# Optimization experiments

Measured on AMD Instinct MI355X. Metric: run time of the kernel, lower is better.

Reference implementation:

```python
import jax, jax.numpy as jnp
import numpy as np

TAU = 1.0
EPS = 1e-06


def setup_inputs() -> dict:
    key = jax.random.key(0)
    batch = jax.random.normal(key, (8192, 256), dtype=jnp.float32)
    return {"batch": batch}


def reference(batch):
    n = batch.shape[0]
    half = n // 2
    # reorder: interleave first half and second half -> [x0, y0, x1, y1, ...]
    idx = jnp.stack([jnp.arange(half), jnp.arange(half) + half], axis=1).reshape(-1)
    x = batch[idx]                                   # [n, d]

    sim = x @ x.T                                    # [n, n] raw dot products
    norm = jnp.linalg.norm(x, axis=1, keepdims=True) # [n, 1]
    normmat = norm @ norm.T                          # [n, n]

    # denominator: zero the diagonal BEFORE exp (diag contributes exp(0)=1, as in torch code)
    mask = 1.0 - jnp.eye(n, dtype=x.dtype)
    den = jnp.sum(jnp.exp(mask * sim / (normmat + EPS) / TAU), axis=1)  # [n]

    # numerator: for row k, positive pair is (i, i+1) with i = 2*(k//2); no eps (faithful)
    i = (jnp.arange(n) // 2) * 2
    num = sim[i, i + 1] / normmat[i, i + 1]          # [n]

    loss = jnp.sum(-jnp.log(jnp.exp(num / TAU) / den)) / n
    return loss
```

## Files before the change

### kernel.cpp

```cpp
#include <hip/hip_runtime.h>
#include <hip/hip_bf16.h>


#define N_ROWS 8192
#define HALF   4096
#define DDIM   256
#define NBLK   64

typedef unsigned int   u32;
typedef unsigned char  u8;
typedef __attribute__((ext_vector_type(4))) float f32x4;
typedef __attribute__((ext_vector_type(4))) int   i32x4;
typedef __attribute__((ext_vector_type(8))) int   i32x8;

__device__ __forceinline__ u32 f2e4m3(float f) {
    const u32 u = __builtin_bit_cast(u32, f);
    const u32 s = (u >> 24) & 0x80u;
    const float af = fabsf(f);
    if (af < 0.015625f) {
        const int mi = (int)rintf(af * 512.0f);
        return s | (u32)mi;
    }
    u32 keep = (u & 0x7FFFFFFFu) >> 20;
    const u32 rem = u & 0xFFFFFu;
    keep += (rem > 0x80000u) || (rem == 0x80000u && (keep & 1u));
    const int ef = (int)(keep >> 3) - 120;
    return s | ((u32)ef << 3) | (keep & 7u);
}

__global__ __launch_bounds__(256) void prep_kernel(const float* __restrict__ x,
                                                   u8* __restrict__ xq,
                                                   float* __restrict__ norms,
                                                   float* __restrict__ dots) {
    const int w = threadIdx.x >> 6, l = threadIdx.x & 63;
    if (blockIdx.x < 2048) {
        const int row = blockIdx.x * 4 + w;
        const float4 v = reinterpret_cast<const float4*>(x + (size_t)row * DDIM)[l];
        float sq = v.x * v.x + v.y * v.y + v.z * v.z + v.w * v.w;
#pragma unroll
        for (int off = 1; off < 64; off <<= 1) sq += __shfl_xor(sq, off);
        const float norm = sqrtf(sq);
        if (l == 0) norms[row] = norm;
        const float rs = 16.0f / norm;
        const u32 pk = f2e4m3(v.x * rs) | (f2e4m3(v.y * rs) << 8) |
                       (f2e4m3(v.z * rs) << 16) | (f2e4m3(v.w * rs) << 24);
        reinterpret_cast<u32*>(xq + (size_t)row * DDIM)[l] = pk;
    } else {
        const int m = (blockIdx.x - 2048) * 4 + w;
        const float4 a = reinterpret_cast<const float4*>(x + (size_t)m * DDIM)[l];
        const float4 b = reinterpret_cast<const float4*>(x + (size_t)(m + HALF) * DDIM)[l];
        float s = a.x * b.x + a.y * b.y + a.z * b.z + a.w * b.w;
#pragma unroll
        for (int off = 1; off < 64; off <<= 1) s += __shfl_xor(s, off);
        if (l == 0) dots[m] = s;
    }
}

__global__ __launch_bounds__(256) void gram_kernel(const u8* __restrict__ xq,
                                                   float* __restrict__ part) {
    const int t = blockIdx.x;
    int bi = (int)(0.5f * (129.0f - sqrtf(16641.0f - 8.0f * (float)t)));
    if (bi > 0 && bi * (129 - bi) / 2 > t) --bi;
    if ((bi + 1) * (129 - (bi + 1)) / 2 <= t) ++bi;
    const int bj = bi + (t - bi * (129 - bi) / 2);
    const bool diagblk = (bi == bj);
    const int r0 = bi * 128, c0 = bj * 128;

    __shared__ __align__(16) char smem[32768];
    u8* As = (u8*)smem;
    u8* Bs = (u8*)(smem + 16384);

    const int tid = threadIdx.x;
    const int w = tid >> 6, l = tid & 63;
    const int wr = w >> 1, wc = w & 1;

    const f32x4 vzero = {0.f, 0.f, 0.f, 0.f};
    f32x4 acc[4][4];
#pragma unroll
    for (int m = 0; m < 4; ++m)
#pragma unroll
        for (int n = 0; n < 4; ++n) acc[m][n] = vzero;

    const int krow = l >> 3;
    const int kbyte = ((l & 7) ^ krow) * 16;
    const int r7 = l & 7;
    const int kq2 = (l >> 4) * 2;

    for (int ks = 0; ks < 2; ++ks) {
#pragma unroll
        for (int i = 0; i < 4; ++i) {
            const int rr = w * 32 + i * 8;
            const u8* ga = xq + (size_t)(r0 + rr + krow) * DDIM + ks * 128 + kbyte;
            __builtin_amdgcn_global_load_lds(
                (const __attribute__((address_space(1))) u32*)ga,
                (__attribute__((address_space(3))) u32*)(As + rr * 128), 16, 0, 0);
            const u8* gb = xq + (size_t)(c0 + rr + krow) * DDIM + ks * 128 + kbyte;
            __builtin_amdgcn_global_load_lds(
                (const __attribute__((address_space(1))) u32*)gb,
                (__attribute__((address_space(3))) u32*)(Bs + rr * 128), 16, 0, 0);
        }
        __syncthreads();

        i32x8 bfr[4];
#pragma unroll
        for (int m = 0; m < 4; ++m) {
            const u8* rowp = Bs + (wc * 64 + m * 16 + (l & 15)) * 128;
            const i32x4 lo = *reinterpret_cast<const i32x4*>(rowp + ((kq2 ^ r7) << 4));
            const i32x4 hi = *reinterpret_cast<const i32x4*>(rowp + (((kq2 + 1) ^ r7) << 4));
            bfr[m][0] = lo[0]; bfr[m][1] = lo[1]; bfr[m][2] = lo[2]; bfr[m][3] = lo[3];
            bfr[m][4] = hi[0]; bfr[m][5] = hi[1]; bfr[m][6] = hi[2]; bfr[m][7] = hi[3];
        }
#pragma unroll
        for (int n = 0; n < 4; ++n) {
            const u8* rowp = As + (wr * 64 + n * 16 + (l & 15)) * 128;
            const i32x4 lo = *reinterpret_cast<const i32x4*>(rowp + ((kq2 ^ r7) << 4));
            const i32x4 hi = *reinterpret_cast<const i32x4*>(rowp + (((kq2 + 1) ^ r7) << 4));
            i32x8 afr;
            afr[0] = lo[0]; afr[1] = lo[1]; afr[2] = lo[2]; afr[3] = lo[3];
            afr[4] = hi[0]; afr[5] = hi[1]; afr[6] = hi[2]; afr[7] = hi[3];
#pragma unroll
            for (int m = 0; m < 4; ++m)
                acc[m][n] = __builtin_amdgcn_mfma_scale_f32_16x16x128_f8f6f4(
                    bfr[m], afr, acc[m][n], 0, 0, 0, 0x7F7F7F7F, 0, 0x7F7F7F7F);
        }
        __syncthreads();
    }

#pragma unroll
    for (int m = 0; m < 4; ++m)
#pragma unroll
        for (int n = 0; n < 4; ++n)
#pragma unroll
            for (int rg = 0; rg < 4; ++rg) {
                const float e = __expf(acc[m][n][rg] * 0.00390625f);
                if (diagblk) {
                    const int j_loc = wc * 64 + m * 16 + (l >> 4) * 4 + rg;
                    const int r_loc = wr * 64 + n * 16 + (l & 15);
                    acc[m][n][rg] = (j_loc == r_loc) ? 1.0f : e;
                } else {
                    acc[m][n][rg] = e;
                }
            }

    float* cs  = (float*)smem;
    float* dsh = (float*)(smem + 24576);

#pragma unroll
    for (int n = 0; n < 4; ++n) {
        float s = 0.f;
#pragma unroll
        for (int m = 0; m < 4; ++m)
#pragma unroll
            for (int rg = 0; rg < 4; ++rg) s += acc[m][n][rg];
        s += __shfl_xor(s, 16);
        s += __shfl_xor(s, 32);
        if (l < 16) dsh[wc * 128 + wr * 64 + n * 16 + l] = s;
    }

    if (!diagblk) {
#pragma unroll
        for (int m = 0; m < 4; ++m)
#pragma unroll
            for (int rg = 0; rg < 4; ++rg) {
                const float s = acc[m][0][rg] + acc[m][1][rg] + acc[m][2][rg] + acc[m][3][rg];
                const int j_loc = wc * 64 + m * 16 + (l >> 4) * 4 + rg;
                cs[(wr * 128 + j_loc) * 17 + (l & 15)] = s;
            }
    }
    __syncthreads();

    if (tid < 128) {
        const float den = dsh[tid] + dsh[128 + tid];
        part[(size_t)bj * N_ROWS + r0 + tid] = den;
        if (!diagblk) {
            float c = 0.f;
#pragma unroll
            for (int k = 0; k < 16; ++k)
                c += cs[tid * 17 + k] + cs[(128 + tid) * 17 + k];
            part[(size_t)bi * N_ROWS + c0 + tid] = c;
        }
    }
}

__global__ __launch_bounds__(256) void fin1_kernel(const float* __restrict__ part,
                                                   const float* __restrict__ norms,
                                                   const float* __restrict__ dots,
                                                   float* __restrict__ bsum) {
    const int b = blockIdx.x, t = threadIdx.x;
    const int r = b * 256 + t;
    float den = 0.f;
#pragma unroll 8
    for (int bj = 0; bj < 64; ++bj) den += part[(size_t)bj * N_ROWS + r];
    float local = logf(den);
    if (t < 128) {
        const int m = b * 128 + t;
        local -= 2.0f * dots[m] / (norms[m] * norms[m + HALF]);
    }
#pragma unroll
    for (int off = 1; off < 64; off <<= 1) local += __shfl_xor(local, off);
    __shared__ float wsum[4];
    if ((t & 63) == 0) wsum[t >> 6] = local;
    __syncthreads();
    if (t == 0) bsum[b] = wsum[0] + wsum[1] + wsum[2] + wsum[3];
}

__global__ void fin2_kernel(const float* __restrict__ bsum, float* __restrict__ out) {
    const int t = threadIdx.x;
    float v = (t < 32) ? bsum[t] : 0.f;
#pragma unroll
    for (int off = 1; off < 32; off <<= 1) v += __shfl_xor(v, off);
    if (t == 0) out[0] = v / (float)N_ROWS;
}

extern "C" void kernel_launch(void* const* d_in, const int* in_sizes, int n_in,
                              void* d_out, int out_size, void* d_ws, size_t ws_size,
                              hipStream_t stream) {
    const float* x = (const float*)d_in[0];
    float* out = (float*)d_out;
    char* ws = (char*)d_ws;

    u8*    xq    = (u8*)ws;
    float* norms = (float*)(ws + 2097152);
    float* dots  = (float*)(ws + 2129920);
    float* part  = (float*)(ws + 2146304);
    float* bsum  = (float*)(ws + 4243456);

    prep_kernel<<<3072, 256, 0, stream>>>(x, xq, norms, dots);
    gram_kernel<<<(NBLK * (NBLK + 1)) / 2, 256, 0, stream>>>(xq, part);
    fin1_kernel<<<32, 256, 0, stream>>>(part, norms, dots, bsum);
    fin2_kernel<<<1, 64, 0, stream>>>(bsum, out);
}
```

Measured before the change: 34.11 us.

## Make gram kernel persistent over tile runs with double-buffered B staging

```diff
diff --git a/kernel.cpp b/kernel.cpp
--- a/kernel.cpp
+++ b/kernel.cpp
@@ -58,127 +58,175 @@
 
 __global__ __launch_bounds__(256) void gram_kernel(const u8* __restrict__ xq,
                                                    float* __restrict__ part) {
-    const int t = blockIdx.x;
-    int bi = (int)(0.5f * (129.0f - sqrtf(16641.0f - 8.0f * (float)t)));
-    if (bi > 0 && bi * (129 - bi) / 2 > t) --bi;
-    if ((bi + 1) * (129 - (bi + 1)) / 2 <= t) ++bi;
-    const int bj = bi + (t - bi * (129 - bi) / 2);
-    const bool diagblk = (bi == bj);
-    const int r0 = bi * 128, c0 = bj * 128;
-
-    __shared__ __align__(16) char smem[32768];
-    u8* As = (u8*)smem;
-    u8* Bs = (u8*)(smem + 16384);
+    const int b = blockIdx.x;
+    int tstart, tcnt;
+    if (b < 32) { tstart = 5 * b;      tcnt = 5; }
+    else        { tstart = 4 * b + 32; tcnt = 4; }
+
+    int bi = (int)(0.5f * (129.0f - sqrtf(16641.0f - 8.0f * (float)tstart)));
+    if (bi > 0 && bi * (129 - bi) / 2 > tstart) --bi;
+    if ((bi + 1) * (129 - (bi + 1)) / 2 <= tstart) ++bi;
+    int bj = bi + (tstart - bi * (129 - bi) / 2);
+
+    __shared__ __align__(16) char smem[51200];
+    float* cs  = (float*)(smem + 32768);
+    float* dsh = (float*)(smem + 32768 + 17408);
 
     const int tid = threadIdx.x;
     const int w = tid >> 6, l = tid & 63;
     const int wr = w >> 1, wc = w & 1;
-
-    const f32x4 vzero = {0.f, 0.f, 0.f, 0.f};
-    f32x4 acc[4][4];
-#pragma unroll
-    for (int m = 0; m < 4; ++m)
-#pragma unroll
-        for (int n = 0; n < 4; ++n) acc[m][n] = vzero;
 
     const int krow = l >> 3;
     const int kbyte = ((l & 7) ^ krow) * 16;
     const int r7 = l & 7;
     const int kq2 = (l >> 4) * 2;
 
-    for (int ks = 0; ks < 2; ++ks) {
+    auto stageB = [&](int c0, int ks, int bufsel) {
 #pragma unroll
         for (int i = 0; i < 4; ++i) {
             const int rr = w * 32 + i * 8;
-            const u8* ga = xq + (size_t)(r0 + rr + krow) * DDIM + ks * 128 + kbyte;
-            __builtin_amdgcn_global_load_lds(
-                (const __attribute__((address_space(1))) u32*)ga,
-                (__attribute__((address_space(3))) u32*)(As + rr * 128), 16, 0, 0);
             const u8* gb = xq + (size_t)(c0 + rr + krow) * DDIM + ks * 128 + kbyte;
             __builtin_amdgcn_global_load_lds(
                 (const __attribute__((address_space(1))) u32*)gb,
-                (__attribute__((address_space(3))) u32*)(Bs + rr * 128), 16, 0, 0);
-        }
+                (__attribute__((address_space(3))) u32*)((u8*)smem + bufsel * 16384 + rr * 128),
+                16, 0, 0);
+        }
+    };
+
+    i32x8 Areg[4][2];
+    f32x4 acc[4][4];
+
+    stageB(bj * 128, 0, 0);
+    int cur = 0;
+    bool newbi = true;
+
+    for (int tt = 0; tt < tcnt; ++tt) {
+        const bool diagblk = (bi == bj);
+        const int r0 = bi * 128, c0 = bj * 128;
+
+        int nbi = bi, nbj = bj + 1;
+        bool nnew = false;
+        if (nbj == NBLK) { nbi = bi + 1; nbj = nbi; nnew = true; }
+        const bool havenext = (tt + 1 < tcnt);
+
+        const f32x4 vzero = {0.f, 0.f, 0.f, 0.f};
+#pragma unroll
+        for (int m = 0; m < 4; ++m)
+#pragma unroll
+            for (int n = 0; n < 4; ++n) acc[m][n] = vzero;
+
         __syncthreads();
-
-        i32x8 bfr[4];
-#pragma unroll
-        for (int m = 0; m < 4; ++m) {
-            const u8* rowp = Bs + (wc * 64 + m * 16 + (l & 15)) * 128;
-            const i32x4 lo = *reinterpret_cast<const i32x4*>(rowp + ((kq2 ^ r7) << 4));
-            const i32x4 hi = *reinterpret_cast<const i32x4*>(rowp + (((kq2 + 1) ^ r7) << 4));
-            bfr[m][0] = lo[0]; bfr[m][1] = lo[1]; bfr[m][2] = lo[2]; bfr[m][3] = lo[3];
-            bfr[m][4] = hi[0]; bfr[m][5] = hi[1]; bfr[m][6] = hi[2]; bfr[m][7] = hi[3];
-        }
+        if (newbi) {
+#pragma unroll
+            for (int n = 0; n < 4; ++n)
+#pragma unroll
+                for (int ks = 0; ks < 2; ++ks) {
+                    const u8* ap = xq + (size_t)(r0 + wr * 64 + n * 16 + (l & 15)) * DDIM
+                                      + ks * 128 + (l >> 4) * 32;
+                    const i32x4 lo = *reinterpret_cast<const i32x4*>(ap);
+                    const i32x4 hi = *reinterpret_cast<const i32x4*>(ap + 16);
+                    Areg[n][ks][0] = lo[0]; Areg[n][ks][1] = lo[1];
+                    Areg[n][ks][2] = lo[2]; Areg[n][ks][3] = lo[3];
+                    Areg[n][ks][4] = hi[0]; Areg[n][ks][5] = hi[1];
+                    Areg[n][ks][6] = hi[2]; Areg[n][ks][7] = hi[3];
+                }
+        }
+        stageB(c0, 1, cur ^ 1);
+        {
+            const u8* Bsrc = (u8*)smem + cur * 16384;
+            i32x8 bfr[4];
+#pragma unroll
+            for (int m = 0; m < 4; ++m) {
+                const u8* rowp = Bsrc + (wc * 64 + m * 16 + (l & 15)) * 128;
+                const i32x4 lo = *reinterpret_cast<const i32x4*>(rowp + ((kq2 ^ r7) << 4));
+                const i32x4 hi = *reinterpret_cast<const i32x4*>(rowp + (((kq2 + 1) ^ r7) << 4));
+                bfr[m][0] = lo[0]; bfr[m][1] = lo[1]; bfr[m][2] = lo[2]; bfr[m][3] = lo[3];
+                bfr[m][4] = hi[0]; bfr[m][5] = hi[1]; bfr[m][6] = hi[2]; bfr[m][7] = hi[3];
+            }
+#pragma unroll
+            for (int n = 0; n < 4; ++n)
+#pragma unroll
+                for (int m = 0; m < 4; ++m)
+                    acc[m][n] = __builtin_amdgcn_mfma_scale_f32_16x16x128_f8f6f4(
+                        bfr[m], Areg[n][0], acc[m][n], 0, 0, 0, 0x7F7F7F7F, 0, 0x7F7F7F7F);
+        }
+        cur ^= 1;
+
+        __syncthreads();
+        if (havenext) stageB(nbj * 128, 0, cur ^ 1);
+        {
+            const u8* Bsrc = (u8*)smem + cur * 16384;
+            i32x8 bfr[4];
+#pragma unroll
+            for (int m = 0; m < 4; ++m) {
+                const u8* rowp = Bsrc + (wc * 64 + m * 16 + (l & 15)) * 128;
+                const i32x4 lo = *reinterpret_cast<const i32x4*>(rowp + ((kq2 ^ r7) << 4));
+                const i32x4 hi = *reinterpret_cast<const i32x4*>(rowp + (((kq2 + 1) ^ r7) << 4));
+                bfr[m][0] = lo[0]; bfr[m][1] = lo[1]; bfr[m][2] = lo[2]; bfr[m][3] = lo[3];
+                bfr[m][4] = hi[0]; bfr[m][5] = hi[1]; bfr[m][6] = hi[2]; bfr[m][7] = hi[3];
+            }
+#pragma unroll
+            for (int n = 0; n < 4; ++n)
+#pragma unroll
+                for (int m = 0; m < 4; ++m)
+                    acc[m][n] = __builtin_amdgcn_mfma_scale_f32_16x16x128_f8f6f4(
+                        bfr[m], Areg[n][1], acc[m][n], 0, 0, 0, 0x7F7F7F7F, 0, 0x7F7F7F7F);
+        }
+        cur ^= 1;
+
+#pragma unroll
+        for (int m = 0; m < 4; ++m)
+#pragma unroll
+            for (int n = 0; n < 4; ++n)
+#pragma unroll
+                for (int rg = 0; rg < 4; ++rg) {
+                    const float e = __expf(acc[m][n][rg] * 0.00390625f);
+                    if (diagblk) {
+                        const int j_loc = wc * 64 + m * 16 + (l >> 4) * 4 + rg;
+                        const int r_loc = wr * 64 + n * 16 + (l & 15);
+                        acc[m][n][rg] = (j_loc == r_loc) ? 1.0f : e;
+                    } else {
+                        acc[m][n][rg] = e;
+                    }
+                }
+
 #pragma unroll
         for (int n = 0; n < 4; ++n) {
-            const u8* rowp = As + (wr * 64 + n * 16 + (l & 15)) * 128;
-            const i32x4 lo = *reinterpret_cast<const i32x4*>(rowp + ((kq2 ^ r7) << 4));
-            const i32x4 hi = *reinterpret_cast<const i32x4*>(rowp + (((kq2 + 1) ^ r7) << 4));
-            i32x8 afr;
-            afr[0] = lo[0]; afr[1] = lo[1]; afr[2] = lo[2]; afr[3] = lo[3];
-            afr[4] = hi[0]; afr[5] = hi[1]; afr[6] = hi[2]; afr[7] = hi[3];
+            float s = 0.f;
 #pragma unroll
             for (int m = 0; m < 4; ++m)
-                acc[m][n] = __builtin_amdgcn_mfma_scale_f32_16x16x128_f8f6f4(
-                    bfr[m], afr, acc[m][n], 0, 0, 0, 0x7F7F7F7F, 0, 0x7F7F7F7F);
+#pragma unroll
+                for (int rg = 0; rg < 4; ++rg) s += acc[m][n][rg];
+            s += __shfl_xor(s, 16);
+            s += __shfl_xor(s, 32);
+            if (l < 16) dsh[wc * 128 + wr * 64 + n * 16 + l] = s;
+        }
+
+        if (!diagblk) {
+#pragma unroll
+            for (int m = 0; m < 4; ++m)
+#pragma unroll
+                for (int rg = 0; rg < 4; ++rg) {
+                    const float s = acc[m][0][rg] + acc[m][1][rg] + acc[m][2][rg] + acc[m][3][rg];
+                    const int j_loc = wc * 64 + m * 16 + (l >> 4) * 4 + rg;
+                    cs[(wr * 128 + j_loc) * 17 + (l & 15)] = s;
+                }
         }
         __syncthreads();
-    }
-
-#pragma unroll
-    for (int m = 0; m < 4; ++m)
-#pragma unroll
-        for (int n = 0; n < 4; ++n)
-#pragma unroll
-            for (int rg = 0; rg < 4; ++rg) {
-                const float e = __expf(acc[m][n][rg] * 0.00390625f);
-                if (diagblk) {
-                    const int j_loc = wc * 64 + m * 16 + (l >> 4) * 4 + rg;
-                    const int r_loc = wr * 64 + n * 16 + (l & 15);
-                    acc[m][n][rg] = (j_loc == r_loc) ? 1.0f : e;
-                } else {
-                    acc[m][n][rg] = e;
-                }
+
+        if (tid < 128) {
+            const float den = dsh[tid] + dsh[128 + tid];
+            part[(size_t)bj * N_ROWS + r0 + tid] = den;
+            if (!diagblk) {
+                float c = 0.f;
+#pragma unroll
+                for (int k = 0; k < 16; ++k)
+                    c += cs[tid * 17 + k] + cs[(128 + tid) * 17 + k];
+                part[(size_t)bi * N_ROWS + c0 + tid] = c;
             }
-
-    float* cs  = (float*)smem;
-    float* dsh = (float*)(smem + 24576);
-
-#pragma unroll
-    for (int n = 0; n < 4; ++n) {
-        float s = 0.f;
-#pragma unroll
-        for (int m = 0; m < 4; ++m)
-#pragma unroll
-            for (int rg = 0; rg < 4; ++rg) s += acc[m][n][rg];
-        s += __shfl_xor(s, 16);
-        s += __shfl_xor(s, 32);
-        if (l < 16) dsh[wc * 128 + wr * 64 + n * 16 + l] = s;
-    }
-
-    if (!diagblk) {
-#pragma unroll
-        for (int m = 0; m < 4; ++m)
-#pragma unroll
-            for (int rg = 0; rg < 4; ++rg) {
-                const float s = acc[m][0][rg] + acc[m][1][rg] + acc[m][2][rg] + acc[m][3][rg];
-                const int j_loc = wc * 64 + m * 16 + (l >> 4) * 4 + rg;
-                cs[(wr * 128 + j_loc) * 17 + (l & 15)] = s;
-            }
-    }
-    __syncthreads();
-
-    if (tid < 128) {
-        const float den = dsh[tid] + dsh[128 + tid];
-        part[(size_t)bj * N_ROWS + r0 + tid] = den;
-        if (!diagblk) {
-            float c = 0.f;
-#pragma unroll
-            for (int k = 0; k < 16; ++k)
-                c += cs[tid * 17 + k] + cs[(128 + tid) * 17 + k];
-            part[(size_t)bi * N_ROWS + c0 + tid] = c;
-        }
+        }
+
+        bi = nbi; bj = nbj; newbi = nnew;
     }
 }
 
@@ -226,7 +274,7 @@
     float* bsum  = (float*)(ws + 4243456);
 
     prep_kernel<<<3072, 256, 0, stream>>>(x, xq, norms, dots);
-    gram_kernel<<<(NBLK * (NBLK + 1)) / 2, 256, 0, stream>>>(xq, part);
+    gram_kernel<<<512, 256, 0, stream>>>(xq, part);
     fin1_kernel<<<32, 256, 0, stream>>>(part, norms, dots, bsum);
     fin2_kernel<<<1, 64, 0, stream>>>(bsum, out);
 }
```

Result: slower. 37.29 us (+9.3%).

## Load MFMA operand fragments directly from global into registers, dropping LDS staging

Applied to the files above, without the earlier changes.

```diff
diff --git a/kernel.cpp b/kernel.cpp
--- a/kernel.cpp
+++ b/kernel.cpp
@@ -66,14 +66,42 @@
     const bool diagblk = (bi == bj);
     const int r0 = bi * 128, c0 = bj * 128;
 
-    __shared__ __align__(16) char smem[32768];
-    u8* As = (u8*)smem;
-    u8* Bs = (u8*)(smem + 16384);
+    __shared__ float cs[2 * 128 * 17];
+    __shared__ float dsh[256];
 
     const int tid = threadIdx.x;
     const int w = tid >> 6, l = tid & 63;
     const int wr = w >> 1, wc = w & 1;
 
+    const u8* abase = xq + (size_t)(r0 + wr * 64 + (l & 15)) * DDIM + (l >> 4) * 32;
+    const u8* bbase = xq + (size_t)(c0 + wc * 64 + (l & 15)) * DDIM + (l >> 4) * 32;
+
+    i32x8 afr[4][2], bfr[4][2];
+#pragma unroll
+    for (int n = 0; n < 4; ++n)
+#pragma unroll
+        for (int ks = 0; ks < 2; ++ks) {
+            const u8* ap = abase + n * 16 * DDIM + ks * 128;
+            const i32x4 lo = *reinterpret_cast<const i32x4*>(ap);
+            const i32x4 hi = *reinterpret_cast<const i32x4*>(ap + 16);
+            afr[n][ks][0] = lo[0]; afr[n][ks][1] = lo[1];
+            afr[n][ks][2] = lo[2]; afr[n][ks][3] = lo[3];
+            afr[n][ks][4] = hi[0]; afr[n][ks][5] = hi[1];
+            afr[n][ks][6] = hi[2]; afr[n][ks][7] = hi[3];
+        }
+#pragma unroll
+    for (int m = 0; m < 4; ++m)
+#pragma unroll
+        for (int ks = 0; ks < 2; ++ks) {
+            const u8* bp = bbase + m * 16 * DDIM + ks * 128;
+            const i32x4 lo = *reinterpret_cast<const i32x4*>(bp);
+            const i32x4 hi = *reinterpret_cast<const i32x4*>(bp + 16);
+            bfr[m][ks][0] = lo[0]; bfr[m][ks][1] = lo[1];
+            bfr[m][ks][2] = lo[2]; bfr[m][ks][3] = lo[3];
+            bfr[m][ks][4] = hi[0]; bfr[m][ks][5] = hi[1];
+            bfr[m][ks][6] = hi[2]; bfr[m][ks][7] = hi[3];
+        }
+
     const f32x4 vzero = {0.f, 0.f, 0.f, 0.f};
     f32x4 acc[4][4];
 #pragma unroll
@@ -81,50 +109,14 @@
 #pragma unroll
         for (int n = 0; n < 4; ++n) acc[m][n] = vzero;
 
-    const int krow = l >> 3;
-    const int kbyte = ((l & 7) ^ krow) * 16;
-    const int r7 = l & 7;
-    const int kq2 = (l >> 4) * 2;
-
-    for (int ks = 0; ks < 2; ++ks) {
-#pragma unroll
-        for (int i = 0; i < 4; ++i) {
-            const int rr = w * 32 + i * 8;
-            const u8* ga = xq + (size_t)(r0 + rr + krow) * DDIM + ks * 128 + kbyte;
-            __builtin_amdgcn_global_load_lds(
-                (const __attribute__((address_space(1))) u32*)ga,
-                (__attribute__((address_space(3))) u32*)(As + rr * 128), 16, 0, 0);
-            const u8* gb = xq + (size_t)(c0 + rr + krow) * DDIM + ks * 128 + kbyte;
-            __builtin_amdgcn_global_load_lds(
-                (const __attribute__((address_space(1))) u32*)gb,
-                (__attribute__((address_space(3))) u32*)(Bs + rr * 128), 16, 0, 0);
-        }
-        __syncthreads();
-
-        i32x8 bfr[4];
-#pragma unroll
-        for (int m = 0; m < 4; ++m) {
-            const u8* rowp = Bs + (wc * 64 + m * 16 + (l & 15)) * 128;
-            const i32x4 lo = *reinterpret_cast<const i32x4*>(rowp + ((kq2 ^ r7) << 4));
-            const i32x4 hi = *reinterpret_cast<const i32x4*>(rowp + (((kq2 + 1) ^ r7) << 4));
-            bfr[m][0] = lo[0]; bfr[m][1] = lo[1]; bfr[m][2] = lo[2]; bfr[m][3] = lo[3];
-            bfr[m][4] = hi[0]; bfr[m][5] = hi[1]; bfr[m][6] = hi[2]; bfr[m][7] = hi[3];
-        }
-#pragma unroll
-        for (int n = 0; n < 4; ++n) {
-            const u8* rowp = As + (wr * 64 + n * 16 + (l & 15)) * 128;
-            const i32x4 lo = *reinterpret_cast<const i32x4*>(rowp + ((kq2 ^ r7) << 4));
-            const i32x4 hi = *reinterpret_cast<const i32x4*>(rowp + (((kq2 + 1) ^ r7) << 4));
-            i32x8 afr;
-            afr[0] = lo[0]; afr[1] = lo[1]; afr[2] = lo[2]; afr[3] = lo[3];
-            afr[4] = hi[0]; afr[5] = hi[1]; afr[6] = hi[2]; afr[7] = hi[3];
+#pragma unroll
+    for (int ks = 0; ks < 2; ++ks)
+#pragma unroll
+        for (int n = 0; n < 4; ++n)
 #pragma unroll
             for (int m = 0; m < 4; ++m)
                 acc[m][n] = __builtin_amdgcn_mfma_scale_f32_16x16x128_f8f6f4(
-                    bfr[m], afr, acc[m][n], 0, 0, 0, 0x7F7F7F7F, 0, 0x7F7F7F7F);
-        }
-        __syncthreads();
-    }
+                    bfr[m][ks], afr[n][ks], acc[m][n], 0, 0, 0, 0x7F7F7F7F, 0, 0x7F7F7F7F);
 
 #pragma unroll
     for (int m = 0; m < 4; ++m)
@@ -141,9 +133,6 @@
                     acc[m][n][rg] = e;
                 }
             }
-
-    float* cs  = (float*)smem;
-    float* dsh = (float*)(smem + 24576);
 
 #pragma unroll
     for (int n = 0; n < 4; ++n) {
```

Measured after the change: 52.08 us. 1.53x slower.

## Double-buffer Gram tile K-panels in LDS to overlap loads with MFMA

Applied to the files above, without the earlier changes.

```diff
diff --git a/kernel.cpp b/kernel.cpp
--- a/kernel.cpp
+++ b/kernel.cpp
@@ -66,45 +66,53 @@
     const bool diagblk = (bi == bj);
     const int r0 = bi * 128, c0 = bj * 128;
 
-    __shared__ __align__(16) char smem[32768];
-    u8* As = (u8*)smem;
-    u8* Bs = (u8*)(smem + 16384);
+    __shared__ __align__(16) u8 smem[65536];
+    u8* const A0 = smem;
+    u8* const A1 = smem + 16384;
+    u8* const B0 = smem + 32768;
+    u8* const B1 = smem + 49152;
 
     const int tid = threadIdx.x;
     const int w = tid >> 6, l = tid & 63;
     const int wr = w >> 1, wc = w & 1;
-
-    const f32x4 vzero = {0.f, 0.f, 0.f, 0.f};
-    f32x4 acc[4][4];
-#pragma unroll
-    for (int m = 0; m < 4; ++m)
-#pragma unroll
-        for (int n = 0; n < 4; ++n) acc[m][n] = vzero;
 
     const int krow = l >> 3;
     const int kbyte = ((l & 7) ^ krow) * 16;
     const int r7 = l & 7;
     const int kq2 = (l >> 4) * 2;
 
-    for (int ks = 0; ks < 2; ++ks) {
+    auto stage = [&](const u8* panel , int ks, u8* dst) {
 #pragma unroll
         for (int i = 0; i < 4; ++i) {
             const int rr = w * 32 + i * 8;
-            const u8* ga = xq + (size_t)(r0 + rr + krow) * DDIM + ks * 128 + kbyte;
+            const u8* g = panel + (size_t)(rr + krow) * DDIM + ks * 128 + kbyte;
             __builtin_amdgcn_global_load_lds(
-                (const __attribute__((address_space(1))) u32*)ga,
-                (__attribute__((address_space(3))) u32*)(As + rr * 128), 16, 0, 0);
-            const u8* gb = xq + (size_t)(c0 + rr + krow) * DDIM + ks * 128 + kbyte;
-            __builtin_amdgcn_global_load_lds(
-                (const __attribute__((address_space(1))) u32*)gb,
-                (__attribute__((address_space(3))) u32*)(Bs + rr * 128), 16, 0, 0);
-        }
-        __syncthreads();
-
-        i32x8 bfr[4];
+                (const __attribute__((address_space(1))) u32*)g,
+                (__attribute__((address_space(3))) u32*)(dst + rr * 128), 16, 0, 0);
+        }
+    };
+
+    const u8* apanel = xq + (size_t)r0 * DDIM;
+    const u8* bpanel = xq + (size_t)c0 * DDIM;
+
+    const f32x4 vzero = {0.f, 0.f, 0.f, 0.f};
+    f32x4 acc[4][4];
+#pragma unroll
+    for (int m = 0; m < 4; ++m)
+#pragma unroll
+        for (int n = 0; n < 4; ++n) acc[m][n] = vzero;
+
+    stage(apanel, 0, A0);
+    stage(apanel, 1, A1);
+    stage(bpanel, 0, B0);
+    __syncthreads();
+
+    stage(bpanel, 1, B1);
+    {
+        i32x8 afr[4], bfr[4];
 #pragma unroll
         for (int m = 0; m < 4; ++m) {
-            const u8* rowp = Bs + (wc * 64 + m * 16 + (l & 15)) * 128;
+            const u8* rowp = B0 + (wc * 64 + m * 16 + (l & 15)) * 128;
             const i32x4 lo = *reinterpret_cast<const i32x4*>(rowp + ((kq2 ^ r7) << 4));
             const i32x4 hi = *reinterpret_cast<const i32x4*>(rowp + (((kq2 + 1) ^ r7) << 4));
             bfr[m][0] = lo[0]; bfr[m][1] = lo[1]; bfr[m][2] = lo[2]; bfr[m][3] = lo[3];
@@ -112,18 +120,45 @@
         }
 #pragma unroll
         for (int n = 0; n < 4; ++n) {
-            const u8* rowp = As + (wr * 64 + n * 16 + (l & 15)) * 128;
-            const i32x4 lo = *reinterpret_cast<const i32x4*>(rowp + ((kq2 ^ r7) << 4));
-            const i32x4 hi = *reinterpret_cast<const i32x4*>(rowp + (((kq2 + 1) ^ r7) << 4));
-            i32x8 afr;
-            afr[0] = lo[0]; afr[1] = lo[1]; afr[2] = lo[2]; afr[3] = lo[3];
-            afr[4] = hi[0]; afr[5] = hi[1]; afr[6] = hi[2]; afr[7] = hi[3];
+            const u8* rowp = A0 + (wr * 64 + n * 16 + (l & 15)) * 128;
+            const i32x4 lo = *reinterpret_cast<const i32x4*>(rowp + ((kq2 ^ r7) << 4));
+            const i32x4 hi = *reinterpret_cast<const i32x4*>(rowp + (((kq2 + 1) ^ r7) << 4));
+            afr[n][0] = lo[0]; afr[n][1] = lo[1]; afr[n][2] = lo[2]; afr[n][3] = lo[3];
+            afr[n][4] = hi[0]; afr[n][5] = hi[1]; afr[n][6] = hi[2]; afr[n][7] = hi[3];
+        }
+#pragma unroll
+        for (int n = 0; n < 4; ++n)
 #pragma unroll
             for (int m = 0; m < 4; ++m)
                 acc[m][n] = __builtin_amdgcn_mfma_scale_f32_16x16x128_f8f6f4(
-                    bfr[m], afr, acc[m][n], 0, 0, 0, 0x7F7F7F7F, 0, 0x7F7F7F7F);
-        }
-        __syncthreads();
+                    bfr[m], afr[n], acc[m][n], 0, 0, 0, 0x7F7F7F7F, 0, 0x7F7F7F7F);
+    }
+    __syncthreads();
+
+    {
+        i32x8 afr[4], bfr[4];
+#pragma unroll
+        for (int m = 0; m < 4; ++m) {
+            const u8* rowp = B1 + (wc * 64 + m * 16 + (l & 15)) * 128;
+            const i32x4 lo = *reinterpret_cast<const i32x4*>(rowp + ((kq2 ^ r7) << 4));
+            const i32x4 hi = *reinterpret_cast<const i32x4*>(rowp + (((kq2 + 1) ^ r7) << 4));
+            bfr[m][0] = lo[0]; bfr[m][1] = lo[1]; bfr[m][2] = lo[2]; bfr[m][3] = lo[3];
+            bfr[m][4] = hi[0]; bfr[m][5] = hi[1]; bfr[m][6] = hi[2]; bfr[m][7] = hi[3];
+        }
+#pragma unroll
+        for (int n = 0; n < 4; ++n) {
+            const u8* rowp = A1 + (wr * 64 + n * 16 + (l & 15)) * 128;
+            const i32x4 lo = *reinterpret_cast<const i32x4*>(rowp + ((kq2 ^ r7) << 4));
+            const i32x4 hi = *reinterpret_cast<const i32x4*>(rowp + (((kq2 + 1) ^ r7) << 4));
+            afr[n][0] = lo[0]; afr[n][1] = lo[1]; afr[n][2] = lo[2]; afr[n][3] = lo[3];
+            afr[n][4] = hi[0]; afr[n][5] = hi[1]; afr[n][6] = hi[2]; afr[n][7] = hi[3];
+        }
+#pragma unroll
+        for (int n = 0; n < 4; ++n)
+#pragma unroll
+            for (int m = 0; m < 4; ++m)
+                acc[m][n] = __builtin_amdgcn_mfma_scale_f32_16x16x128_f8f6f4(
+                    bfr[m], afr[n], acc[m][n], 0, 0, 0, 0x7F7F7F7F, 0, 0x7F7F7F7F);
     }
 
 #pragma unroll
@@ -142,8 +177,10 @@
                 }
             }
 
+    __syncthreads();
+
     float* cs  = (float*)smem;
-    float* dsh = (float*)(smem + 24576);
+    float* dsh = (float*)(smem + 20480);
 
 #pragma unroll
     for (int n = 0; n < 4; ++n) {
```

After: 37.09 us. 1.09x slower.
